# Kernel tuning notes

Measured on AMD Instinct MI355X. Metric: run time of the kernel, lower is better.

The kernel has to match this reference:

```python
import jax, jax.numpy as jnp
import numpy as np

B, S, T = 4096, 2048, 2  # batch of conversations, turns per conversation, num_tags


def setup_inputs() -> dict:
    key = jax.random.key(0)
    k1, k2, k3, k4, k5, k6 = jax.random.split(key, 6)
    emissions = jax.random.normal(k1, (B, S, T), dtype=jnp.float32)
    # learned transition matrices for DistanceCRF branch order:
    # [even2odd, I0, D_consecutive, D_nonconsecutive]
    trans_params = jax.random.normal(k2, (4, T, T), dtype=jnp.float32) * 0.1
    tags = jax.random.randint(k3, (B, S), 0, T)
    who2who = jax.random.randint(k4, (B, S), 0, 2)
    intime = jax.random.randint(k5, (B, S), 0, 3)
    distance = jax.random.randint(k6, (B, S), 0, 4)
    return {"emissions": emissions, "trans_params": trans_params, "tags": tags,
            "who2who": who2who, "intime": intime, "distance": distance}


def _select_trans(trans_params, who2who, intime, distance):
    """Per-step transition matrix selection (DistanceCRF logic).
    Returns [B, S, T, T]."""
    Tn = trans_params.shape[-1]
    # index 0 = zero 'padding' matrix (who2who == -1 case)
    bank = jnp.concatenate([jnp.zeros((1, Tn, Tn), trans_params.dtype), trans_params], axis=0)
    sel = jnp.where(who2who == -1, 0,
          jnp.where(who2who == 1, 1,          # even2odd
          jnp.where(intime == 0, 2,           # I0
          jnp.where(distance == 0, 3, 4))))   # D_consecutive / D_nonconsecutive
    return bank[sel]


def reference(emissions, trans_params, tags, who2who, intime, distance):
    Bn, Sn, Tn = emissions.shape
    trans = _select_trans(trans_params, who2who, intime, distance)  # [B,S,T,T]

    # ---- gold path score ----
    em_gold = jnp.take_along_axis(emissions, tags[..., None], axis=-1)[..., 0].sum(-1)  # [B]
    oh_prev = jax.nn.one_hot(tags[:, :-1], Tn, dtype=emissions.dtype)  # [B,S-1,T]
    oh_cur = jax.nn.one_hot(tags[:, 1:], Tn, dtype=emissions.dtype)
    tr_gold = jnp.einsum('bsij,bsi,bsj->b', trans[:, 1:], oh_prev, oh_cur)  # [B]
    gold_score = em_gold + tr_gold

    # ---- log partition via forward recursion (note: transition added at t=0 too,
    # matching the original implementation) ----
    def step(alpha, xs):
        em_t, tr_t = xs  # [B,T], [B,T,T]
        new_alpha = jax.nn.logsumexp(alpha[:, :, None] + em_t[:, None, :] + tr_t, axis=1)
        return new_alpha, None

    alpha0 = jnp.zeros((Bn, Tn), emissions.dtype)
    xs = (jnp.swapaxes(emissions, 0, 1), jnp.swapaxes(trans, 0, 1))  # [S,B,T], [S,B,T,T]
    alpha, _ = jax.lax.scan(step, alpha0, xs)
    total_score = jax.nn.logsumexp(alpha, axis=-1)  # [B]

    return jnp.stack([gold_score, total_score])  # [2, B]
```

## Files before the change

kernel.cpp:

```cpp
#include <hip/hip_runtime.h>
#include <math.h>

#define Bn 4096
#define Sn 2048
#define BLOCK 256
#define CHUNK (Sn / BLOCK)
#define NM (Bn * BLOCK)

__global__ __launch_bounds__(BLOCK) void crf_chunk(
    const float* __restrict__ emissions,
    const float* __restrict__ trans_params,
    const int*   __restrict__ tags,
    const int*   __restrict__ who2who,
    const int*   __restrict__ intime,
    const int*   __restrict__ distance,
    float2*      __restrict__ wsA,
    float2*      __restrict__ wsB,
    float2*      __restrict__ wsC)
{
    const int b = blockIdx.x;
    const int c = threadIdx.x;
    const long base = (long)b * Sn;
    const int s0 = c * CHUNK;

    __shared__ __align__(16) float lbank[20];
    __shared__ __align__(16) float ebank[20];

    const int4* tp = (const int4*)(tags     + base) + c * 2;
    const int4* wp = (const int4*)(who2who  + base) + c * 2;
    const int4* ip = (const int4*)(intime   + base) + c * 2;
    const int4* dp = (const int4*)(distance + base) + c * 2;
    const float4* ep = (const float4*)(emissions + base * 2) + c * 4;

    float4 e0 = ep[0], e1 = ep[1], e2 = ep[2], e3 = ep[3];
    int4 ta = tp[0], tb = tp[1];
    int4 wa = wp[0], wb = wp[1];
    int4 ia = ip[0], ib = ip[1];
    int4 da = dp[0], db = dp[1];
    int prev_tag = (c > 0) ? tags[base + s0 - 1] : 0;

    if (c < 20) {
        float v = (c < 4) ? 0.0f : trans_params[c - 4];
        lbank[c] = v;
        ebank[c] = __expf(v);
    }
    __syncthreads();

    int wv[CHUNK]   = {wa.x, wa.y, wa.z, wa.w, wb.x, wb.y, wb.z, wb.w};
    int iv[CHUNK]   = {ia.x, ia.y, ia.z, ia.w, ib.x, ib.y, ib.z, ib.w};
    int dv[CHUNK]   = {da.x, da.y, da.z, da.w, db.x, db.y, db.z, db.w};
    int tagv[CHUNK] = {ta.x, ta.y, ta.z, ta.w, tb.x, tb.y, tb.z, tb.w};
    float emv[CHUNK][2] = {
        {e0.x, e0.y}, {e0.z, e0.w}, {e1.x, e1.y}, {e1.z, e1.w},
        {e2.x, e2.y}, {e2.z, e2.w}, {e3.x, e3.y}, {e3.z, e3.w}};

    int sel[CHUNK];
    #pragma unroll
    for (int k = 0; k < CHUNK; ++k) {
        int w = wv[k], it = iv[k], d = dv[k];
        sel[k] = (w == -1) ? 0 : (w == 1) ? 1 : (it == 0) ? 2 : (d == 0) ? 3 : 4;
    }

    float4 P0 = *(const float4*)(ebank + sel[0] * 4);
    float m00 = P0.x * __expf(emv[0][0]), m01 = P0.y * __expf(emv[0][1]);
    float m10 = P0.z * __expf(emv[0][0]), m11 = P0.w * __expf(emv[0][1]);
    #pragma unroll
    for (int k = 1; k < CHUNK; ++k) {
        float4 P = *(const float4*)(ebank + sel[k] * 4);
        float x0 = __expf(emv[k][0]), x1 = __expf(emv[k][1]);
        float n00 = fmaf(m00, P.x, m01 * P.z) * x0;
        float n01 = fmaf(m00, P.y, m01 * P.w) * x1;
        float n10 = fmaf(m10, P.x, m11 * P.z) * x0;
        float n11 = fmaf(m10, P.y, m11 * P.w) * x1;
        m00 = n00; m01 = n01; m10 = n10; m11 = n11;
    }

    float gold = 0.0f;
    #pragma unroll
    for (int k = 0; k < CHUNK; ++k) {
        int tg = tagv[k];
        gold += tg ? emv[k][1] : emv[k][0];
        if (k > 0 || c > 0) {
            int pt = (k == 0) ? prev_tag : tagv[k - 1];
            gold += lbank[(sel[k] << 2) + (pt << 1) + tg];
        }
    }

    float mx  = fmaxf(fmaxf(m00, m01), fmaxf(m10, m11));
    float inv = 1.0f / mx;
    float L   = __logf(mx);

    const int gid = b * BLOCK + c;
    wsA[gid] = make_float2(m00 * inv, m01 * inv);
    wsB[gid] = make_float2(m10 * inv, m11 * inv);
    wsC[gid] = make_float2(L, gold);
}

__global__ __launch_bounds__(BLOCK) void crf_reduce(
    const float2* __restrict__ wsA,
    const float2* __restrict__ wsB,
    const float2* __restrict__ wsC,
    float*        __restrict__ out)
{
    const int lane = threadIdx.x & 63;
    const int wave = threadIdx.x >> 6;
    const int b = blockIdx.x * 4 + wave;

    const int idx4 = b * (BLOCK / 2) + lane * 2;
    const float4* A4 = (const float4*)wsA;
    const float4* B4 = (const float4*)wsB;
    const float4* C4 = (const float4*)wsC;
    float4 a0 = A4[idx4], a1 = A4[idx4 + 1];
    float4 b0 = B4[idx4], b1 = B4[idx4 + 1];
    float4 c0 = C4[idx4], c1 = C4[idx4 + 1];

    float m00 = a0.x, m01 = a0.y, m10 = b0.x, m11 = b0.y;
    float L = c0.x, gold = c0.y;
    {
        float q00[3] = {a0.z, a1.x, a1.z};
        float q01[3] = {a0.w, a1.y, a1.w};
        float q10[3] = {b0.z, b1.x, b1.z};
        float q11[3] = {b0.w, b1.y, b1.w};
        float qL[3]  = {c0.z, c1.x, c1.z};
        float qg[3]  = {c0.w, c1.y, c1.w};
        #pragma unroll
        for (int q = 0; q < 3; ++q) {
            float n00 = fmaf(m00, q00[q], m01 * q10[q]);
            float n01 = fmaf(m00, q01[q], m01 * q11[q]);
            float n10 = fmaf(m10, q00[q], m11 * q10[q]);
            float n11 = fmaf(m10, q01[q], m11 * q11[q]);
            m00 = n00; m01 = n01; m10 = n10; m11 = n11;
            L += qL[q]; gold += qg[q];
        }
        float mx  = fmaxf(fmaxf(m00, m01), fmaxf(m10, m11));
        float inv = 1.0f / mx;
        L += __logf(mx);
        m00 *= inv; m01 *= inv; m10 *= inv; m11 *= inv;
    }

    #pragma unroll
    for (int m = 1; m < 64; m <<= 1) {
        float o00 = __shfl_xor(m00, m);
        float o01 = __shfl_xor(m01, m);
        float o10 = __shfl_xor(m10, m);
        float o11 = __shfl_xor(m11, m);
        float oL  = __shfl_xor(L, m);
        float og  = __shfl_xor(gold, m);
        bool up = (lane & m) != 0;
        float x00 = up ? o00 : m00, x01 = up ? o01 : m01;
        float x10 = up ? o10 : m10, x11 = up ? o11 : m11;
        float y00 = up ? m00 : o00, y01 = up ? m01 : o01;
        float y10 = up ? m10 : o10, y11 = up ? m11 : o11;
        m00 = fmaf(x00, y00, x01 * y10);
        m01 = fmaf(x00, y01, x01 * y11);
        m10 = fmaf(x10, y00, x11 * y10);
        m11 = fmaf(x10, y01, x11 * y11);
        L += oL;
        gold += og;
        float mx  = fmaxf(fmaxf(m00, m01), fmaxf(m10, m11));
        float inv = 1.0f / mx;
        L += __logf(mx);
        m00 *= inv; m01 *= inv; m10 *= inv; m11 *= inv;
    }

    if (lane == 0) {
        float tot = L + __logf(m00 + m01 + m10 + m11);
        out[b]      = gold;
        out[Bn + b] = tot;
    }
}

extern "C" void kernel_launch(void* const* d_in, const int* in_sizes, int n_in,
                              void* d_out, int out_size, void* d_ws, size_t ws_size,
                              hipStream_t stream) {
    const float* emissions    = (const float*)d_in[0];
    const float* trans_params = (const float*)d_in[1];
    const int*   tags         = (const int*)d_in[2];
    const int*   who2who      = (const int*)d_in[3];
    const int*   intime       = (const int*)d_in[4];
    const int*   distance     = (const int*)d_in[5];
    float* out = (float*)d_out;

    float2* wsA = (float2*)d_ws;
    float2* wsB = wsA + NM;
    float2* wsC = wsB + NM;

    crf_chunk<<<dim3(Bn), dim3(BLOCK), 0, stream>>>(
        emissions, trans_params, tags, who2who, intime, distance,
        wsA, wsB, wsC);
    crf_reduce<<<dim3(Bn / 4), dim3(BLOCK), 0, stream>>>(
        wsA, wsB, wsC, out);
}
```

Measured before the change: 213.0 us.

## Make chunk kernel persistent with register double-buffered prefetch of next sequence

The chunk kernel now launches a fixed grid where each block loops over several conversations, loading the next conversation's inputs into registers while it processes the current one, with scheduling barriers that keep the prefetch ahead of compute. The previous-tag lookup is replaced by a wave shuffle, leaving a global load only at wave boundaries. The aim is to hide global load latency and cut per-block launch and setup cost in a bandwidth-bound kernel. The cost is higher register pressure from holding two sets of inputs, and fewer resident blocks, which may reduce the latency hiding that occupancy used to provide.

```diff
diff --git a/kernel.cpp b/kernel.cpp
--- a/kernel.cpp
+++ b/kernel.cpp
@@ -5,9 +5,39 @@
 #define Sn 2048
 #define BLOCK 256
 #define CHUNK (Sn / BLOCK)
+#define GRID 1024
+#define ITERS (Bn / GRID)
 #define NM (Bn * BLOCK)
 
-__global__ __launch_bounds__(BLOCK) void crf_chunk(
+struct SeqRegs {
+    float4 e0, e1, e2, e3;
+    int4 ta, tb, wa, wb, ia, ib, da, db;
+    int ptag;
+};
+
+__device__ __forceinline__ SeqRegs load_seq(
+    const float* __restrict__ em, const int* __restrict__ tg,
+    const int* __restrict__ wh, const int* __restrict__ it,
+    const int* __restrict__ ds, int b, int t)
+{
+    SeqRegs r;
+    const long base = (long)b * Sn;
+    const float4* ep = (const float4*)(em + base * 2) + t * 4;
+    const int4* tp = (const int4*)(tg + base) + t * 2;
+    const int4* wp = (const int4*)(wh + base) + t * 2;
+    const int4* ip = (const int4*)(it + base) + t * 2;
+    const int4* dp = (const int4*)(ds + base) + t * 2;
+    r.e0 = ep[0]; r.e1 = ep[1]; r.e2 = ep[2]; r.e3 = ep[3];
+    r.ta = tp[0]; r.tb = tp[1];
+    r.wa = wp[0]; r.wb = wp[1];
+    r.ia = ip[0]; r.ib = ip[1];
+    r.da = dp[0]; r.db = dp[1];
+    r.ptag = 0;
+    if ((t & 63) == 0 && t > 0) r.ptag = tg[base + t * CHUNK - 1];
+    return r;
+}
+
+__global__ __launch_bounds__(BLOCK, 3) void crf_chunk(
     const float* __restrict__ emissions,
     const float* __restrict__ trans_params,
     const int*   __restrict__ tags,
@@ -18,82 +48,91 @@
     float2*      __restrict__ wsB,
     float2*      __restrict__ wsC)
 {
-    const int b = blockIdx.x;
-    const int c = threadIdx.x;
-    const long base = (long)b * Sn;
-    const int s0 = c * CHUNK;
+    const int t = threadIdx.x;
 
     __shared__ __align__(16) float lbank[20];
     __shared__ __align__(16) float ebank[20];
-
-    const int4* tp = (const int4*)(tags     + base) + c * 2;
-    const int4* wp = (const int4*)(who2who  + base) + c * 2;
-    const int4* ip = (const int4*)(intime   + base) + c * 2;
-    const int4* dp = (const int4*)(distance + base) + c * 2;
-    const float4* ep = (const float4*)(emissions + base * 2) + c * 4;
-
-    float4 e0 = ep[0], e1 = ep[1], e2 = ep[2], e3 = ep[3];
-    int4 ta = tp[0], tb = tp[1];
-    int4 wa = wp[0], wb = wp[1];
-    int4 ia = ip[0], ib = ip[1];
-    int4 da = dp[0], db = dp[1];
-    int prev_tag = (c > 0) ? tags[base + s0 - 1] : 0;
-
-    if (c < 20) {
-        float v = (c < 4) ? 0.0f : trans_params[c - 4];
-        lbank[c] = v;
-        ebank[c] = __expf(v);
+    if (t < 20) {
+        float v = (t < 4) ? 0.0f : trans_params[t - 4];
+        lbank[t] = v;
+        ebank[t] = __expf(v);
     }
     __syncthreads();
 
-    int wv[CHUNK]   = {wa.x, wa.y, wa.z, wa.w, wb.x, wb.y, wb.z, wb.w};
-    int iv[CHUNK]   = {ia.x, ia.y, ia.z, ia.w, ib.x, ib.y, ib.z, ib.w};
-    int dv[CHUNK]   = {da.x, da.y, da.z, da.w, db.x, db.y, db.z, db.w};
-    int tagv[CHUNK] = {ta.x, ta.y, ta.z, ta.w, tb.x, tb.y, tb.z, tb.w};
-    float emv[CHUNK][2] = {
-        {e0.x, e0.y}, {e0.z, e0.w}, {e1.x, e1.y}, {e1.z, e1.w},
-        {e2.x, e2.y}, {e2.z, e2.w}, {e3.x, e3.y}, {e3.z, e3.w}};
-
-    int sel[CHUNK];
+    auto process = [&](const SeqRegs& r, int b) {
+        int tagv[CHUNK] = {r.ta.x, r.ta.y, r.ta.z, r.ta.w,
+                           r.tb.x, r.tb.y, r.tb.z, r.tb.w};
+        int wv[CHUNK]   = {r.wa.x, r.wa.y, r.wa.z, r.wa.w,
+                           r.wb.x, r.wb.y, r.wb.z, r.wb.w};
+        int iv[CHUNK]   = {r.ia.x, r.ia.y, r.ia.z, r.ia.w,
+                           r.ib.x, r.ib.y, r.ib.z, r.ib.w};
+        int dv[CHUNK]   = {r.da.x, r.da.y, r.da.z, r.da.w,
+                           r.db.x, r.db.y, r.db.z, r.db.w};
+        float emv[CHUNK][2] = {
+            {r.e0.x, r.e0.y}, {r.e0.z, r.e0.w}, {r.e1.x, r.e1.y},
+            {r.e1.z, r.e1.w}, {r.e2.x, r.e2.y}, {r.e2.z, r.e2.w},
+            {r.e3.x, r.e3.y}, {r.e3.z, r.e3.w}};
+
+        int pt0 = __shfl_up(tagv[CHUNK - 1], 1);
+        if ((t & 63) == 0) pt0 = r.ptag;
+
+        int sel[CHUNK];
+        #pragma unroll
+        for (int k = 0; k < CHUNK; ++k) {
+            int w = wv[k], it2 = iv[k], d = dv[k];
+            sel[k] = (w == -1) ? 0 : (w == 1) ? 1
+                   : (it2 == 0) ? 2 : (d == 0) ? 3 : 4;
+        }
+
+        float4 P0 = *(const float4*)(ebank + sel[0] * 4);
+        float x00 = __expf(emv[0][0]), x01 = __expf(emv[0][1]);
+        float m00 = P0.x * x00, m01 = P0.y * x01;
+        float m10 = P0.z * x00, m11 = P0.w * x01;
+        #pragma unroll
+        for (int k = 1; k < CHUNK; ++k) {
+            float4 P = *(const float4*)(ebank + sel[k] * 4);
+            float x0 = __expf(emv[k][0]), x1 = __expf(emv[k][1]);
+            float n00 = fmaf(m00, P.x, m01 * P.z) * x0;
+            float n01 = fmaf(m00, P.y, m01 * P.w) * x1;
+            float n10 = fmaf(m10, P.x, m11 * P.z) * x0;
+            float n11 = fmaf(m10, P.y, m11 * P.w) * x1;
+            m00 = n00; m01 = n01; m10 = n10; m11 = n11;
+        }
+
+        float gold = 0.0f;
+        #pragma unroll
+        for (int k = 0; k < CHUNK; ++k) {
+            int tg = tagv[k];
+            gold += tg ? emv[k][1] : emv[k][0];
+            if (k > 0 || t > 0) {
+                int pt = (k == 0) ? pt0 : tagv[k - 1];
+                gold += lbank[(sel[k] << 2) + (pt << 1) + tg];
+            }
+        }
+
+        float mx  = fmaxf(fmaxf(m00, m01), fmaxf(m10, m11));
+        float inv = 1.0f / mx;
+        float L   = __logf(mx);
+        const int gid = b * BLOCK + t;
+        wsA[gid] = make_float2(m00 * inv, m01 * inv);
+        wsB[gid] = make_float2(m10 * inv, m11 * inv);
+        wsC[gid] = make_float2(L, gold);
+    };
+
+    int b = blockIdx.x;
+    SeqRegs cur = load_seq(emissions, tags, who2who, intime, distance, b, t);
     #pragma unroll
-    for (int k = 0; k < CHUNK; ++k) {
-        int w = wv[k], it = iv[k], d = dv[k];
-        sel[k] = (w == -1) ? 0 : (w == 1) ? 1 : (it == 0) ? 2 : (d == 0) ? 3 : 4;
-    }
-
-    float4 P0 = *(const float4*)(ebank + sel[0] * 4);
-    float m00 = P0.x * __expf(emv[0][0]), m01 = P0.y * __expf(emv[0][1]);
-    float m10 = P0.z * __expf(emv[0][0]), m11 = P0.w * __expf(emv[0][1]);
-    #pragma unroll
-    for (int k = 1; k < CHUNK; ++k) {
-        float4 P = *(const float4*)(ebank + sel[k] * 4);
-        float x0 = __expf(emv[k][0]), x1 = __expf(emv[k][1]);
-        float n00 = fmaf(m00, P.x, m01 * P.z) * x0;
-        float n01 = fmaf(m00, P.y, m01 * P.w) * x1;
-        float n10 = fmaf(m10, P.x, m11 * P.z) * x0;
-        float n11 = fmaf(m10, P.y, m11 * P.w) * x1;
-        m00 = n00; m01 = n01; m10 = n10; m11 = n11;
-    }
-
-    float gold = 0.0f;
-    #pragma unroll
-    for (int k = 0; k < CHUNK; ++k) {
-        int tg = tagv[k];
-        gold += tg ? emv[k][1] : emv[k][0];
-        if (k > 0 || c > 0) {
-            int pt = (k == 0) ? prev_tag : tagv[k - 1];
-            gold += lbank[(sel[k] << 2) + (pt << 1) + tg];
-        }
-    }
-
-    float mx  = fmaxf(fmaxf(m00, m01), fmaxf(m10, m11));
-    float inv = 1.0f / mx;
-    float L   = __logf(mx);
-
-    const int gid = b * BLOCK + c;
-    wsA[gid] = make_float2(m00 * inv, m01 * inv);
-    wsB[gid] = make_float2(m10 * inv, m11 * inv);
-    wsC[gid] = make_float2(L, gold);
+    for (int itr = 0; itr < ITERS; ++itr) {
+        SeqRegs nxt;
+        if (itr + 1 < ITERS)
+            nxt = load_seq(emissions, tags, who2who, intime, distance,
+                           b + GRID, t);
+        __builtin_amdgcn_sched_barrier(0);
+        process(cur, b);
+        __builtin_amdgcn_sched_barrier(0);
+        cur = nxt;
+        b += GRID;
+    }
 }
 
 __global__ __launch_bounds__(BLOCK) void crf_reduce(
@@ -185,7 +224,7 @@
     float2* wsB = wsA + NM;
     float2* wsC = wsB + NM;
 
-    crf_chunk<<<dim3(Bn), dim3(BLOCK), 0, stream>>>(
+    crf_chunk<<<dim3(GRID), dim3(BLOCK), 0, stream>>>(
         emissions, trans_params, tags, who2who, intime, distance,
         wsA, wsB, wsC);
     crf_reduce<<<dim3(Bn / 4), dim3(BLOCK), 0, stream>>>(
```

New measurement: 214.1 us. Within noise of the previous version (+0.5%).
